# Optimization experiments

Measured on AMD Instinct MI355X. Metric: run time of the kernel, lower is better.

## Reference

```python
import jax, jax.numpy as jnp
import numpy as np

B, S, D, DFF = 8, 2048, 1024, 4096

def setup_inputs() -> dict:
    key = jax.random.key(0)
    ks = jax.random.split(key, 11)
    s = 0.02
    return {
        "x":  jax.random.normal(ks[0], (B, S, D), dtype=jnp.float32),
        "Wq": jax.random.normal(ks[1], (D, D), dtype=jnp.float32) * s,
        "bq": jnp.zeros((D,), dtype=jnp.float32),
        "Wk": jax.random.normal(ks[2], (D, D), dtype=jnp.float32) * s,
        "bk": jnp.zeros((D,), dtype=jnp.float32),
        "Wv": jax.random.normal(ks[3], (D, D), dtype=jnp.float32) * s,
        "bv": jnp.zeros((D,), dtype=jnp.float32),
        "W1": jax.random.normal(ks[4], (DFF, D), dtype=jnp.float32) * s,
        "b1": jnp.zeros((DFF,), dtype=jnp.float32),
        "W2": jax.random.normal(ks[5], (D, DFF), dtype=jnp.float32) * s,
        "b2": jnp.zeros((D,), dtype=jnp.float32),
    }

def reference(x, Wq, bq, Wk, bk, Wv, bv, W1, b1, W2, b2):
    # qkv projections (torch Linear: x @ W.T + b)
    q = jnp.einsum('bsd,ed->bse', x, Wq) + bq
    k = jnp.einsum('bsd,ed->bse', x, Wk) + bk
    v = jnp.einsum('bsd,ed->bse', x, Wv) + bv
    # single-head scaled dot-product attention with causal mask (decoder=True)
    scale = 1.0 / jnp.sqrt(jnp.asarray(q.shape[-1], q.dtype))
    scores = jnp.einsum('bqd,bkd->bqk', q, k) * scale  # (B,S,S)
    causal = jnp.tril(jnp.ones((scores.shape[-2], scores.shape[-1]), dtype=bool))
    scores = jnp.where(causal, scores, jnp.asarray(-jnp.inf, scores.dtype))
    attn = jax.nn.softmax(scores, axis=-1)
    attn_out = jnp.einsum('bqk,bkd->bqd', attn, v)
    # MLP: linear_2(gelu(linear_1(.)))  — exact (erf) GELU as in torch default
    h = jax.nn.gelu(jnp.einsum('bsd,fd->bsf', attn_out, W1) + b1, approximate=False)
    return jnp.einsum('bsf,df->bsd', h, W2) + b2
```

## Files before the change

kernel.cpp:

```cpp
#include <hip/hip_runtime.h>
#include <hip/hip_bf16.h>

#define NB   8
#define SS   2048
#define DD   1024
#define DFFN 4096
#define MTOT (NB*SS)

typedef unsigned short u16;
typedef __attribute__((ext_vector_type(4))) float f32x4;
typedef __attribute__((ext_vector_type(8))) short bf16x8;
typedef __attribute__((ext_vector_type(4))) int i32x4;
typedef __attribute__((ext_vector_type(4))) unsigned short u16x4;
typedef __attribute__((ext_vector_type(8))) unsigned short u16x8;

__device__ __forceinline__ u16 f2bf(float f) {
  union { float f; unsigned u; } c; c.f = f;
  unsigned r = c.u + 0x7FFFu + ((c.u >> 16) & 1u);
  return (u16)(r >> 16);
}

__device__ __forceinline__ void gload16(const void* g, void* l) {
  __builtin_amdgcn_global_load_lds(
      (const __attribute__((address_space(1))) void*)(unsigned long long)g,
      (__attribute__((address_space(3))) void*)(unsigned)(unsigned long long)l,
      16, 0, 0);
}

__device__ __forceinline__ bf16x8 dsr128(unsigned addr) {
  i32x4 r;
  asm volatile("ds_read_b128 %0, %1" : "=v"(r) : "v"(addr));
  return __builtin_bit_cast(bf16x8, r);
}

template<int EBIAS, int EGELU, int ESCALE, int EROWSCALE, int OUTMODE, int CSKIP, int CK>
__global__ __launch_bounds__(256, 3)
void gemm128(const u16* __restrict__ A, const u16* __restrict__ B,
             const float* __restrict__ bias0, const float* __restrict__ bias1,
             const float* __restrict__ bias2, const float* __restrict__ rowscale,
             void* __restrict__ C0, void* __restrict__ C1, void* __restrict__ C2,
             int K, int lda, int ldb, int ldc, float scale,
             long long sA, long long sB, long long sC, int sRS)
{
  __shared__ __align__(1024) u16 smem[16384];

  const int nwg = gridDim.x * gridDim.y;
  const int orig = blockIdx.y * gridDim.x + blockIdx.x;
  const int q = nwg >> 3, r = nwg & 7;
  const int xcd = orig & 7, pos0 = orig >> 3;
  const int wg = (xcd < r ? xcd * (q + 1) : r * (q + 1) + (xcd - r) * q) + pos0;
  const int bx = wg % gridDim.x, by = wg / gridDim.x;
  const int row0 = by * 128, col0 = bx * 128;
  if (CSKIP && col0 > row0 + 127) return;

  const int z = blockIdx.z;
  A += (size_t)z * sA;
  B += (size_t)z * sB;

  int nkt = K >> 5;
  if (CK) { int lim = (row0 + 128) >> 5; if (lim < nkt) nkt = lim; }

  const int tid  = threadIdx.x;
  const int wid  = tid >> 6;
  const int lane = tid & 63;
  const int wr = wid >> 1, wc = wid & 1;

  const int srow = wid * 16 + (lane >> 2);
  const int sunit = (lane & 3) ^ ((lane >> 3) & 3);
  const char* gA = (const char*)A + ((size_t)(row0 + srow) * lda + sunit * 8) * 2;
  const char* gB = (const char*)B + ((size_t)(col0 + srow) * ldb + sunit * 8) * 2;
  const size_t ldab = (size_t)64 * lda * 2;
  const size_t ldbb = (size_t)64 * ldb * 2;

  #define STG(t2) { char* lb = (char*)smem + ((t2) & 1) * 16384; size_t kb = (size_t)(t2) * 64; \
      gload16(gA + kb,        lb + wid * 1024);                                                 \
      gload16(gA + kb + ldab, lb + 4096 + wid * 1024);                                          \
      gload16(gB + kb,        lb + 8192 + wid * 1024);                                          \
      gload16(gB + kb + ldbb, lb + 8192 + 4096 + wid * 1024); }

  const int fr = lane & 15;
  const int ks16 = ((lane >> 4) & 3) * 16;
  const int xm = ((lane >> 1) & 3) << 4;
  const unsigned sbase = (unsigned)(unsigned long long)(void*)smem;

  f32x4 acc[4][4] = {};

  STG(0);
  asm volatile("s_waitcnt vmcnt(0)");
  asm volatile("s_barrier" ::: "memory");

  for (int t = 0; t < nkt; ++t) {
    if (t + 1 < nkt) STG(t + 1);
    const unsigned cb = sbase + (t & 1) * 16384;
    bf16x8 af[4], bf[4];
#pragma unroll
    for (int m = 0; m < 4; ++m)
      af[m] = dsr128(cb + (((wr * 64 + m * 16 + fr) * 64 + ks16) ^ xm));
#pragma unroll
    for (int n = 0; n < 4; ++n)
      bf[n] = dsr128(cb + ((8192 + (wc * 64 + n * 16 + fr) * 64 + ks16) ^ xm));
    asm volatile("s_waitcnt lgkmcnt(0)");
    __builtin_amdgcn_sched_barrier(0);
    __builtin_amdgcn_s_setprio(1);
#pragma unroll
    for (int m = 0; m < 4; ++m)
#pragma unroll
      for (int n = 0; n < 4; ++n)
        acc[m][n] = __builtin_amdgcn_mfma_f32_16x16x32_bf16(af[m], bf[n], acc[m][n], 0, 0, 0);
    __builtin_amdgcn_s_setprio(0);
    asm volatile("s_waitcnt vmcnt(0)");
    asm volatile("s_barrier" ::: "memory");
  }
  #undef STG

  char* sm = (char*)smem;
  const int r4 = (lane >> 4) * 4;
  const int sel  = (OUTMODE == 3) ? (col0 >> 10) : 0;
  const int oc0  = (OUTMODE == 3) ? (col0 & 1023) : col0;
  const float* bias = (OUTMODE == 3) ? (sel == 0 ? bias0 : sel == 1 ? bias1 : bias2)
                                     : bias0;

  if (OUTMODE == 1) {
#pragma unroll
    for (int p = 0; p < 2; ++p) {
      if (wc == p) {
#pragma unroll
        for (int n = 0; n < 4; ++n) {
          const int col = oc0 + wc * 64 + n * 16 + fr;
          const int pb = (n * 16 + fr) * 4;
          float bia = EBIAS ? bias[col] : 0.0f;
#pragma unroll
          for (int m = 0; m < 4; ++m) {
#pragma unroll
            for (int j = 0; j < 4; ++j) {
              const int line = wr * 64 + m * 16 + r4 + j;
              float xv = acc[m][n][j];
              if (EBIAS)     xv += bia;
              if (ESCALE)    xv *= scale;
              if (EROWSCALE) xv *= rowscale[z * sRS + row0 + line];
              if (EGELU)     xv = 0.5f * xv * (1.0f + erff(xv * 0.70710678118f));
              *(float*)(sm + ((line * 256 + pb) ^ ((line & 7) << 4))) = xv;
            }
          }
        }
      }
      __syncthreads();
      float* Cb = (float*)C0 + (size_t)z * sC;
#pragma unroll
      for (int i = 0; i < 8; ++i) {
        const int o = i * 4096 + tid * 16;
        const int line = o >> 8, ps = o & 255;
        f32x4 v = *(const f32x4*)(sm + ((line * 256 + ps) ^ ((line & 7) << 4)));
        *(f32x4*)((char*)(Cb + (size_t)(row0 + line) * ldc + oc0 + p * 64) + ps) = v;
      }
      __syncthreads();
    }
  } else if (OUTMODE == 3 && sel == 2) {
#pragma unroll
    for (int n = 0; n < 4; ++n) {
      const int line = wc * 64 + n * 16 + fr;
      float bia = EBIAS ? bias[oc0 + line] : 0.0f;
#pragma unroll
      for (int m = 0; m < 4; ++m) {
        const int rb = wr * 64 + m * 16 + r4;
        u16x4 pk;
#pragma unroll
        for (int j = 0; j < 4; ++j) pk[j] = f2bf(acc[m][n][j] + bia);
        *(u16x4*)(sm + ((line * 256 + rb * 2) ^ ((line & 7) << 4))) = pk;
      }
    }
    __syncthreads();
    u16* Cb = (u16*)C2 + (size_t)(row0 >> 11) * (DD * SS) + (row0 & (SS - 1));
#pragma unroll
    for (int i = 0; i < 8; ++i) {
      const int o = i * 4096 + tid * 16;
      const int line = o >> 8, ps = o & 255;
      f32x4 v = *(const f32x4*)(sm + ((line * 256 + ps) ^ ((line & 7) << 4)));
      *(f32x4*)((char*)(Cb + (size_t)(oc0 + line) * SS) + ps) = v;
    }
  } else {
#pragma unroll
    for (int n = 0; n < 4; ++n) {
      const int col = oc0 + wc * 64 + n * 16 + fr;
      const int pc = (wc * 64 + n * 16 + fr) * 2;
      float bia = EBIAS ? bias[col] : 0.0f;
#pragma unroll
      for (int m = 0; m < 4; ++m) {
#pragma unroll
        for (int j = 0; j < 4; ++j) {
          const int line = wr * 64 + m * 16 + r4 + j;
          float xv = acc[m][n][j];
          if (EBIAS)     xv += bia;
          if (ESCALE)    xv *= scale;
          if (EROWSCALE) xv *= rowscale[z * sRS + row0 + line];
          if (EGELU)     xv = 0.5f * xv * (1.0f + erff(xv * 0.70710678118f));
          u16 u;
          if (OUTMODE == 2) { union { u16 s; _Float16 h; } cu; cu.h = (_Float16)xv; u = cu.s; }
          else u = f2bf(xv);
          *(u16*)(sm + ((line * 256 + pc) ^ ((line & 7) << 4))) = u;
        }
      }
    }
    __syncthreads();
    u16* Cb = (u16*)(OUTMODE == 3 ? (sel ? C1 : C0) : C0) + (size_t)z * sC + oc0;
#pragma unroll
    for (int i = 0; i < 8; ++i) {
      const int o = i * 4096 + tid * 16;
      const int line = o >> 8, ps = o & 255;
      f32x4 v = *(const f32x4*)(sm + ((line * 256 + ps) ^ ((line & 7) << 4)));
      *(f32x4*)((char*)(Cb + (size_t)(row0 + line) * ldc) + ps) = v;
    }
  }
}

template<int EBIAS, int EGELU, int OUTF32>
__global__ __launch_bounds__(128, 2)
void gemm128w(const u16* __restrict__ A, const u16* __restrict__ B,
              const float* __restrict__ bias, void* __restrict__ C,
              int K, int lda, int ldb, int ldc)
{
  __shared__ __align__(1024) u16 smem[16384];

  const int nwg = gridDim.x * gridDim.y;
  const int orig = blockIdx.y * gridDim.x + blockIdx.x;
  const int q = nwg >> 3, r = nwg & 7;
  const int xcd = orig & 7, pos0 = orig >> 3;
  const int wg = (xcd < r ? xcd * (q + 1) : r * (q + 1) + (xcd - r) * q) + pos0;
  const int bx = wg % gridDim.x, by = wg / gridDim.x;
  const int row0 = by * 128, col0 = bx * 128;

  const int nkt = K >> 5;
  const int tid = threadIdx.x, wid = tid >> 6, lane = tid & 63;
  const int fr = lane & 15;
  const int ks16 = ((lane >> 4) & 3) * 16;
  const int xm = ((lane >> 1) & 3) << 4;
  const int sunit = (lane & 3) ^ ((lane >> 3) & 3);
  const char* gA = (const char*)A + ((size_t)(row0 + wid * 64 + (lane >> 2)) * lda + sunit * 8) * 2;
  const char* gB = (const char*)B + ((size_t)(col0 + wid * 64 + (lane >> 2)) * ldb + sunit * 8) * 2;
  const size_t ldab = (size_t)16 * lda * 2, ldbb = (size_t)16 * ldb * 2;
  const unsigned sbase = (unsigned)(unsigned long long)(void*)smem;

  #define STGW(t2) { char* lb = (char*)smem + ((t2) & 1) * 16384; size_t kb = (size_t)(t2) * 64; \
      char* la = lb + wid * 4096; char* lbb = lb + 8192 + wid * 4096;                            \
      gload16(gA + kb,            la);                                                            \
      gload16(gA + kb +     ldab, la + 1024);                                                     \
      gload16(gA + kb + 2 * ldab, la + 2048);                                                     \
      gload16(gA + kb + 3 * ldab, la + 3072);                                                     \
      gload16(gB + kb,            lbb);                                                           \
      gload16(gB + kb +     ldbb, lbb + 1024);                                                    \
      gload16(gB + kb + 2 * ldbb, lbb + 2048);                                                    \
      gload16(gB + kb + 3 * ldbb, lbb + 3072); }

  f32x4 acc[8][4] = {};

  STGW(0);
  asm volatile("s_waitcnt vmcnt(0)");
  asm volatile("s_barrier" ::: "memory");

  for (int t = 0; t < nkt; ++t) {
    if (t + 1 < nkt) STGW(t + 1);
    const unsigned cb = sbase + (t & 1) * 16384;
    bf16x8 af[8], bf[4];
#pragma unroll
    for (int m = 0; m < 8; ++m)
      af[m] = dsr128(cb + (((m * 16 + fr) * 64 + ks16) ^ xm));
#pragma unroll
    for (int n = 0; n < 4; ++n)
      bf[n] = dsr128(cb + ((8192 + (wid * 64 + n * 16 + fr) * 64 + ks16) ^ xm));
    asm volatile("s_waitcnt lgkmcnt(0)");
    __builtin_amdgcn_sched_barrier(0);
    __builtin_amdgcn_s_setprio(1);
#pragma unroll
    for (int m = 0; m < 8; ++m)
#pragma unroll
      for (int n = 0; n < 4; ++n)
        acc[m][n] = __builtin_amdgcn_mfma_f32_16x16x32_bf16(af[m], bf[n], acc[m][n], 0, 0, 0);
    __builtin_amdgcn_s_setprio(0);
    asm volatile("s_waitcnt vmcnt(0)");
    asm volatile("s_barrier" ::: "memory");
  }
  #undef STGW

  char* sm = (char*)smem;
  const int r4 = (lane >> 4) * 4;

  if (OUTF32) {
#pragma unroll
    for (int p = 0; p < 2; ++p) {
      if (wid == p) {
#pragma unroll
        for (int n = 0; n < 4; ++n) {
          const int col = col0 + wid * 64 + n * 16 + fr;
          const int pb = (n * 16 + fr) * 4;
          float bia = EBIAS ? bias[col] : 0.0f;
#pragma unroll
          for (int m = 0; m < 8; ++m) {
#pragma unroll
            for (int j = 0; j < 4; ++j) {
              const int line = m * 16 + r4 + j;
              float xv = acc[m][n][j] + bia;
              if (EGELU) xv = 0.5f * xv * (1.0f + erff(xv * 0.70710678118f));
              *(float*)(sm + ((line * 256 + pb) ^ ((line & 7) << 4))) = xv;
            }
          }
        }
      }
      __syncthreads();
#pragma unroll
      for (int i = 0; i < 16; ++i) {
        const int o = i * 2048 + tid * 16;
        const int line = o >> 8, ps = o & 255;
        f32x4 v = *(const f32x4*)(sm + ((line * 256 + ps) ^ ((line & 7) << 4)));
        *(f32x4*)((char*)((float*)C + (size_t)(row0 + line) * ldc + col0 + p * 64) + ps) = v;
      }
      __syncthreads();
    }
  } else {
#pragma unroll
    for (int n = 0; n < 4; ++n) {
      const int col = col0 + wid * 64 + n * 16 + fr;
      const int pc = (wid * 64 + n * 16 + fr) * 2;
      float bia = EBIAS ? bias[col] : 0.0f;
#pragma unroll
      for (int m = 0; m < 8; ++m) {
#pragma unroll
        for (int j = 0; j < 4; ++j) {
          const int line = m * 16 + r4 + j;
          float xv = acc[m][n][j] + bia;
          if (EGELU) xv = 0.5f * xv * (1.0f + erff(xv * 0.70710678118f));
          *(u16*)(sm + ((line * 256 + pc) ^ ((line & 7) << 4))) = f2bf(xv);
        }
      }
    }
    __syncthreads();
#pragma unroll
    for (int i = 0; i < 16; ++i) {
      const int o = i * 2048 + tid * 16;
      const int line = o >> 8, ps = o & 255;
      f32x4 v = *(const f32x4*)(sm + ((line * 256 + ps) ^ ((line & 7) << 4)));
      *(f32x4*)((char*)((u16*)C + (size_t)(row0 + line) * ldc) + col0 * 2 + ps) = v;
    }
  }
}

__global__ __launch_bounds__(256) void cvt_bf16_k(const float* __restrict__ in, u16* __restrict__ out, int n4) {
  int i = blockIdx.x * blockDim.x + threadIdx.x;
  if (i < n4) {
    float4 v = ((const float4*)in)[i];
    u16x4 o;
    o.x = f2bf(v.x); o.y = f2bf(v.y); o.z = f2bf(v.z); o.w = f2bf(v.w);
    ((u16x4*)out)[i] = o;
  }
}

__global__ __launch_bounds__(256) void softmax_k(u16* __restrict__ sc, float* __restrict__ rinv, int rows0) {
  const int widx = blockIdx.x * 4 + (threadIdx.x >> 6);
  const int lane = threadIdx.x & 63;
  u16* row = sc + (size_t)widx * SS;
  const int L = (widx & (SS - 1)) + 1;
  float mx = -1e30f;
  for (int k = 0; k < 4; ++k) {
    const int j0 = k * 512 + lane * 8;
    if (j0 < L) {
      u16x8 v = *(const u16x8*)(row + j0);
      int lim = L - j0; if (lim > 8) lim = 8;
#pragma unroll
      for (int e = 0; e < 8; ++e) {
        if (e < lim) { union { u16 u; _Float16 h; } c; c.u = v[e]; mx = fmaxf(mx, (float)c.h); }
      }
    }
  }
#pragma unroll
  for (int o = 32; o >= 1; o >>= 1) mx = fmaxf(mx, __shfl_xor(mx, o));
  float s = 0.0f;
  for (int k = 0; k < 4; ++k) {
    const int j0 = k * 512 + lane * 8;
    u16x8 v = *(const u16x8*)(row + j0);
    u16x8 w;
#pragma unroll
    for (int e = 0; e < 8; ++e) {
      const int j = j0 + e;
      float ev = 0.0f;
      if (j < L) { union { u16 u; _Float16 h; } c; c.u = v[e]; ev = __expf((float)c.h - mx); s += ev; }
      w[e] = f2bf(ev);
    }
    *(u16x8*)(row + j0) = w;
  }
#pragma unroll
  for (int o = 32; o >= 1; o >>= 1) s += __shfl_xor(s, o);
  if (lane == 0) rinv[rows0 + widx] = 1.0f / s;
}

extern "C" void kernel_launch(void* const* d_in, const int* in_sizes, int n_in,
                              void* d_out, int out_size, void* d_ws, size_t ws_size,
                              hipStream_t stream) {
  const float* x  = (const float*)d_in[0];
  const float* Wq = (const float*)d_in[1];
  const float* bq = (const float*)d_in[2];
  const float* Wk = (const float*)d_in[3];
  const float* bk = (const float*)d_in[4];
  const float* Wv = (const float*)d_in[5];
  const float* bv = (const float*)d_in[6];
  const float* W1 = (const float*)d_in[7];
  const float* b1 = (const float*)d_in[8];
  const float* W2 = (const float*)d_in[9];
  const float* b2 = (const float*)d_in[10];

  char* ws = (char*)d_ws;
  u16*  xb   = (u16*)(ws);
  u16*  Wcat = (u16*)(ws + 33554432);
  u16*  W1b  = (u16*)(ws + 39845888);
  u16*  W2b  = (u16*)(ws + 48234496);
  u16*  Qb   = (u16*)(ws + 56623104);
  u16*  Kb   = (u16*)(ws + 90177536);
  u16*  Vtb  = (u16*)(ws + 123731968);
  float* rinv = (float*)(ws + 157286400);
  u16*  big  = (u16*)(ws + 157351936);
  u16*  att  = xb;

  const size_t base = 157351936ull;
  const size_t avail = ws_size > base ? ws_size - base : 0;
  int GB = 8; while (GB > 1 && (size_t)GB * 8388608ull > avail) GB >>= 1;
  int MC = 8192; while (MC > 2048 && (size_t)MC * 8192ull > avail) MC >>= 1;

  cvt_bf16_k<<<MTOT * DD / 4 / 256, 256, 0, stream>>>(x, xb, MTOT * DD / 4);
  cvt_bf16_k<<<DD * DD / 4 / 256, 256, 0, stream>>>(Wq, Wcat, DD * DD / 4);
  cvt_bf16_k<<<DD * DD / 4 / 256, 256, 0, stream>>>(Wk, Wcat + DD * DD, DD * DD / 4);
  cvt_bf16_k<<<DD * DD / 4 / 256, 256, 0, stream>>>(Wv, Wcat + 2 * DD * DD, DD * DD / 4);
  cvt_bf16_k<<<DFFN * DD / 4 / 256, 256, 0, stream>>>(W1, W1b, DFFN * DD / 4);
  cvt_bf16_k<<<DFFN * DD / 4 / 256, 256, 0, stream>>>(W2, W2b, DFFN * DD / 4);

  gemm128<1,0,0,0,3,0,0><<<dim3(3 * DD / 128, MTOT / 128), 256, 0, stream>>>(
      xb, Wcat, bq, bk, bv, nullptr, (void*)Qb, (void*)Kb, (void*)Vtb,
      DD, DD, DD, DD, 0.f, 0, 0, 0, 0);

  for (int b0 = 0; b0 < NB; b0 += GB) {
    gemm128<0,0,1,0,2,1,0><<<dim3(SS/128, SS/128, GB), 256, 0, stream>>>(
        Qb + (size_t)b0 * SS * DD, Kb + (size_t)b0 * SS * DD,
        nullptr, nullptr, nullptr, nullptr, (void*)big, nullptr, nullptr,
        DD, DD, DD, SS, 0.03125f,
        (long long)SS * DD, (long long)SS * DD, (long long)SS * SS, 0);
    softmax_k<<<GB * SS / 4, 256, 0, stream>>>(big, rinv, b0 * SS);
    gemm128<0,0,0,1,0,0,1><<<dim3(DD/128, SS/128, GB), 256, 0, stream>>>(
        big, Vtb + (size_t)b0 * DD * SS,
        nullptr, nullptr, nullptr, rinv + (size_t)b0 * SS,
        (void*)(att + (size_t)b0 * SS * DD), nullptr, nullptr,
        SS, SS, SS, DD, 0.f,
        (long long)SS * SS, (long long)DD * SS, (long long)SS * DD, SS);
  }

  for (int c = 0; c < MTOT / MC; ++c) {
    u16* h = big;
    gemm128w<1,1,0><<<dim3(DFFN/128, MC/128), 128, 0, stream>>>(
        att + (size_t)c * MC * DD, W1b, b1, (void*)h, DD, DD, DD, DFFN);
    gemm128w<1,0,1><<<dim3(DD/128, MC/128), 128, 0, stream>>>(
        h, W2b, b2, (void*)((float*)d_out + (size_t)c * MC * DD), DFFN, DFFN, DFFN, DD);
  }
}
```

Before: 829.5 us.

## Shrink MLP GEMM tile to 128x64 with per-wave private LDS pipelines

The MLP GEMM kernel now uses a 128x64 output tile. Each of its two waves owns a 64x64 sub-tile and its own double-buffered LDS region, so the block-wide barriers are replaced by per-wave vmcnt waits. The epilogue is also written per wave without __syncthreads. Launch bounds rise to 3 blocks per CU, and the MLP chunk size can double so fewer chunks are launched. The aim is to remove barrier stalls and raise occupancy, at the cost of less operand reuse per tile (B is reloaded by each wave) and more global traffic.

```diff
diff --git a/kernel.cpp b/kernel.cpp
--- a/kernel.cpp
+++ b/kernel.cpp
@@ -214,10 +214,10 @@
 }
 
 template<int EBIAS, int EGELU, int OUTF32>
-__global__ __launch_bounds__(128, 2)
-void gemm128w(const u16* __restrict__ A, const u16* __restrict__ B,
-              const float* __restrict__ bias, void* __restrict__ C,
-              int K, int lda, int ldb, int ldc)
+__global__ __launch_bounds__(128, 3)
+void gemmw(const u16* __restrict__ A, const u16* __restrict__ B,
+           const float* __restrict__ bias, void* __restrict__ C,
+           int K, int lda, int ldb, int ldc)
 {
   __shared__ __align__(1024) u16 smem[16384];
 
@@ -227,118 +227,113 @@
   const int xcd = orig & 7, pos0 = orig >> 3;
   const int wg = (xcd < r ? xcd * (q + 1) : r * (q + 1) + (xcd - r) * q) + pos0;
   const int bx = wg % gridDim.x, by = wg / gridDim.x;
-  const int row0 = by * 128, col0 = bx * 128;
+  const int row0 = by * 128, col0 = bx * 64;
 
   const int nkt = K >> 5;
   const int tid = threadIdx.x, wid = tid >> 6, lane = tid & 63;
+  const int rw0 = row0 + wid * 64;
   const int fr = lane & 15;
   const int ks16 = ((lane >> 4) & 3) * 16;
   const int xm = ((lane >> 1) & 3) << 4;
   const int sunit = (lane & 3) ^ ((lane >> 3) & 3);
-  const char* gA = (const char*)A + ((size_t)(row0 + wid * 64 + (lane >> 2)) * lda + sunit * 8) * 2;
-  const char* gB = (const char*)B + ((size_t)(col0 + wid * 64 + (lane >> 2)) * ldb + sunit * 8) * 2;
-  const size_t ldab = (size_t)16 * lda * 2, ldbb = (size_t)16 * ldb * 2;
+
+  const char* gA = (const char*)A + ((size_t)(rw0 + (lane >> 2)) * lda + sunit * 8) * 2;
+  const char* gB = (const char*)B + ((size_t)(col0 + (lane >> 2)) * ldb + sunit * 8) * 2;
+  const size_t ldab = (size_t)16 * lda * 2;
+  const size_t ldbb = (size_t)16 * ldb * 2;
+  char* sm = (char*)smem;
+  const unsigned wb = wid * 16384;
   const unsigned sbase = (unsigned)(unsigned long long)(void*)smem;
 
-  #define STGW(t2) { char* lb = (char*)smem + ((t2) & 1) * 16384; size_t kb = (size_t)(t2) * 64; \
-      char* la = lb + wid * 4096; char* lbb = lb + 8192 + wid * 4096;                            \
-      gload16(gA + kb,            la);                                                            \
-      gload16(gA + kb +     ldab, la + 1024);                                                     \
-      gload16(gA + kb + 2 * ldab, la + 2048);                                                     \
-      gload16(gA + kb + 3 * ldab, la + 3072);                                                     \
-      gload16(gB + kb,            lbb);                                                           \
-      gload16(gB + kb +     ldbb, lbb + 1024);                                                    \
-      gload16(gB + kb + 2 * ldbb, lbb + 2048);                                                    \
-      gload16(gB + kb + 3 * ldbb, lbb + 3072); }
-
-  f32x4 acc[8][4] = {};
+  #define STGW(t2) { char* lb = sm + wb + ((t2) & 1) * 8192; size_t kb = (size_t)(t2) * 64; \
+      gload16(gA + kb,            lb);                                                      \
+      gload16(gA + kb +     ldab, lb + 1024);                                               \
+      gload16(gA + kb + 2 * ldab, lb + 2048);                                               \
+      gload16(gA + kb + 3 * ldab, lb + 3072);                                               \
+      gload16(gB + kb,            lb + 4096);                                               \
+      gload16(gB + kb +     ldbb, lb + 5120);                                               \
+      gload16(gB + kb + 2 * ldbb, lb + 6144);                                               \
+      gload16(gB + kb + 3 * ldbb, lb + 7168); }
+
+  f32x4 acc[4][4] = {};
 
   STGW(0);
-  asm volatile("s_waitcnt vmcnt(0)");
-  asm volatile("s_barrier" ::: "memory");
-
   for (int t = 0; t < nkt; ++t) {
-    if (t + 1 < nkt) STGW(t + 1);
-    const unsigned cb = sbase + (t & 1) * 16384;
-    bf16x8 af[8], bf[4];
-#pragma unroll
-    for (int m = 0; m < 8; ++m)
+    if (t + 1 < nkt) {
+      STGW(t + 1);
+      asm volatile("s_waitcnt vmcnt(8)" ::: "memory");
+    } else {
+      asm volatile("s_waitcnt vmcnt(0)" ::: "memory");
+    }
+    const unsigned cb = sbase + wb + (t & 1) * 8192;
+    bf16x8 af[4], bf[4];
+#pragma unroll
+    for (int m = 0; m < 4; ++m)
       af[m] = dsr128(cb + (((m * 16 + fr) * 64 + ks16) ^ xm));
 #pragma unroll
     for (int n = 0; n < 4; ++n)
-      bf[n] = dsr128(cb + ((8192 + (wid * 64 + n * 16 + fr) * 64 + ks16) ^ xm));
-    asm volatile("s_waitcnt lgkmcnt(0)");
+      bf[n] = dsr128(cb + ((4096 + (n * 16 + fr) * 64 + ks16) ^ xm));
+    asm volatile("s_waitcnt lgkmcnt(0)" ::: "memory");
     __builtin_amdgcn_sched_barrier(0);
     __builtin_amdgcn_s_setprio(1);
 #pragma unroll
-    for (int m = 0; m < 8; ++m)
+    for (int m = 0; m < 4; ++m)
 #pragma unroll
       for (int n = 0; n < 4; ++n)
         acc[m][n] = __builtin_amdgcn_mfma_f32_16x16x32_bf16(af[m], bf[n], acc[m][n], 0, 0, 0);
     __builtin_amdgcn_s_setprio(0);
-    asm volatile("s_waitcnt vmcnt(0)");
-    asm volatile("s_barrier" ::: "memory");
   }
   #undef STGW
 
-  char* sm = (char*)smem;
   const int r4 = (lane >> 4) * 4;
 
   if (OUTF32) {
 #pragma unroll
-    for (int p = 0; p < 2; ++p) {
-      if (wid == p) {
-#pragma unroll
-        for (int n = 0; n < 4; ++n) {
-          const int col = col0 + wid * 64 + n * 16 + fr;
-          const int pb = (n * 16 + fr) * 4;
-          float bia = EBIAS ? bias[col] : 0.0f;
-#pragma unroll
-          for (int m = 0; m < 8; ++m) {
-#pragma unroll
-            for (int j = 0; j < 4; ++j) {
-              const int line = m * 16 + r4 + j;
-              float xv = acc[m][n][j] + bia;
-              if (EGELU) xv = 0.5f * xv * (1.0f + erff(xv * 0.70710678118f));
-              *(float*)(sm + ((line * 256 + pb) ^ ((line & 7) << 4))) = xv;
-            }
-          }
-        }
-      }
-      __syncthreads();
-#pragma unroll
-      for (int i = 0; i < 16; ++i) {
-        const int o = i * 2048 + tid * 16;
-        const int line = o >> 8, ps = o & 255;
-        f32x4 v = *(const f32x4*)(sm + ((line * 256 + ps) ^ ((line & 7) << 4)));
-        *(f32x4*)((char*)((float*)C + (size_t)(row0 + line) * ldc + col0 + p * 64) + ps) = v;
-      }
-      __syncthreads();
-    }
-  } else {
-#pragma unroll
     for (int n = 0; n < 4; ++n) {
-      const int col = col0 + wid * 64 + n * 16 + fr;
-      const int pc = (wid * 64 + n * 16 + fr) * 2;
+      const int col = col0 + n * 16 + fr;
+      const int pb = (n * 16 + fr) * 4;
       float bia = EBIAS ? bias[col] : 0.0f;
 #pragma unroll
-      for (int m = 0; m < 8; ++m) {
+      for (int m = 0; m < 4; ++m) {
 #pragma unroll
         for (int j = 0; j < 4; ++j) {
           const int line = m * 16 + r4 + j;
           float xv = acc[m][n][j] + bia;
           if (EGELU) xv = 0.5f * xv * (1.0f + erff(xv * 0.70710678118f));
-          *(u16*)(sm + ((line * 256 + pc) ^ ((line & 7) << 4))) = f2bf(xv);
+          *(float*)(sm + wb + ((line * 256 + pb) ^ ((line & 7) << 4))) = xv;
         }
       }
     }
-    __syncthreads();
 #pragma unroll
     for (int i = 0; i < 16; ++i) {
-      const int o = i * 2048 + tid * 16;
+      const int o = i * 1024 + lane * 16;
       const int line = o >> 8, ps = o & 255;
-      f32x4 v = *(const f32x4*)(sm + ((line * 256 + ps) ^ ((line & 7) << 4)));
-      *(f32x4*)((char*)((u16*)C + (size_t)(row0 + line) * ldc) + col0 * 2 + ps) = v;
+      f32x4 v = *(const f32x4*)(sm + wb + ((line * 256 + ps) ^ ((line & 7) << 4)));
+      *(f32x4*)((char*)C + ((size_t)(rw0 + line) * ldc + col0) * 4 + ps) = v;
+    }
+  } else {
+#pragma unroll
+    for (int n = 0; n < 4; ++n) {
+      const int col = col0 + n * 16 + fr;
+      const int pc = (n * 16 + fr) * 2;
+      float bia = EBIAS ? bias[col] : 0.0f;
+#pragma unroll
+      for (int m = 0; m < 4; ++m) {
+#pragma unroll
+        for (int j = 0; j < 4; ++j) {
+          const int line = m * 16 + r4 + j;
+          float xv = acc[m][n][j] + bia;
+          if (EGELU) xv = 0.5f * xv * (1.0f + erff(xv * 0.70710678118f));
+          *(u16*)(sm + wb + ((line * 128 + pc) ^ ((line & 7) << 4))) = f2bf(xv);
+        }
+      }
+    }
+#pragma unroll
+    for (int i = 0; i < 8; ++i) {
+      const int o = i * 1024 + lane * 16;
+      const int line = o >> 7, ps = o & 127;
+      f32x4 v = *(const f32x4*)(sm + wb + ((line * 128 + ps) ^ ((line & 7) << 4)));
+      *(f32x4*)((char*)C + ((size_t)(rw0 + line) * ldc + col0) * 2 + ps) = v;
     }
   }
 }
@@ -421,7 +416,7 @@
   const size_t base = 157351936ull;
   const size_t avail = ws_size > base ? ws_size - base : 0;
   int GB = 8; while (GB > 1 && (size_t)GB * 8388608ull > avail) GB >>= 1;
-  int MC = 8192; while (MC > 2048 && (size_t)MC * 8192ull > avail) MC >>= 1;
+  int MC = 16384; while (MC > 2048 && (size_t)MC * 8192ull > avail) MC >>= 1;
 
   cvt_bf16_k<<<MTOT * DD / 4 / 256, 256, 0, stream>>>(x, xb, MTOT * DD / 4);
   cvt_bf16_k<<<DD * DD / 4 / 256, 256, 0, stream>>>(Wq, Wcat, DD * DD / 4);
@@ -451,9 +446,9 @@
 
   for (int c = 0; c < MTOT / MC; ++c) {
     u16* h = big;
-    gemm128w<1,1,0><<<dim3(DFFN/128, MC/128), 128, 0, stream>>>(
+    gemmw<1,1,0><<<dim3(DFFN/64, MC/128), 128, 0, stream>>>(
         att + (size_t)c * MC * DD, W1b, b1, (void*)h, DD, DD, DD, DFFN);
-    gemm128w<1,0,1><<<dim3(DD/128, MC/128), 128, 0, stream>>>(
+    gemmw<1,0,1><<<dim3(DD/64, MC/128), 128, 0, stream>>>(
         h, W2b, b2, (void*)((float*)d_out + (size_t)c * MC * DD), DFFN, DFFN, DFFN, DD);
   }
 }
```

After: 938.0 us. +13.1%, slower.
